# Kernel optimization log

Measured on AMD Instinct MI355X. Metric: run time of the kernel, lower is better.

The kernel has to match this reference:

```python
import math
import jax, jax.numpy as jnp
import numpy as np

DIM = 256
HEADS = 8
WS = (8, 8)   # window_size
SS = (4, 4)   # shift_size


def _rel_tables():
    """Static SwinV2 continuous relative-position coordinate table and index."""
    wh, ww = WS
    ch = np.arange(-(wh - 1), wh, dtype=np.float32)
    cw = np.arange(-(ww - 1), ww, dtype=np.float32)
    table = np.stack(np.meshgrid(ch, cw, indexing='ij'), axis=-1)  # (2wh-1, 2ww-1, 2)
    table[..., 0] /= (wh - 1)
    table[..., 1] /= (ww - 1)
    table *= 8.0
    table = np.sign(table) * np.log2(np.abs(table) + 1.0) / 3.0
    coords = np.stack(np.meshgrid(np.arange(wh), np.arange(ww), indexing='ij'))
    cf = coords.reshape(2, -1)                      # (2, N)
    rel = (cf[:, :, None] - cf[:, None, :]).transpose(1, 2, 0)  # (N, N, 2)
    rel[..., 0] += wh - 1
    rel[..., 1] += ww - 1
    rel[..., 0] *= 2 * ww - 1
    idx = rel.sum(-1).reshape(-1)                   # (N*N,)
    return jnp.asarray(table, jnp.float32), jnp.asarray(idx, jnp.int32)


def _attn_mask(pad_H, pad_W, sh, sw):
    """Static shifted-window attention mask, shape (num_windows, N, N)."""
    wh, ww = WS
    m = np.zeros((pad_H, pad_W), np.float32)
    cnt = 0
    for hs in ((0, -wh), (-wh, -sh), (-sh, None)):
        for ws_ in ((0, -ww), (-ww, -sw), (-sw, None)):
            m[hs[0]:hs[1], ws_[0]:ws_[1]] = cnt
            cnt += 1
    m = m.reshape(pad_H // wh, wh, pad_W // ww, ww).transpose(0, 2, 1, 3)
    m = m.reshape(-1, wh * ww)                      # (nW, N)
    diff = m[:, None, :] - m[:, :, None]            # (nW, N, N)
    return jnp.asarray(np.where(diff != 0, -100.0, 0.0).astype(np.float32))


def setup_inputs() -> dict:
    key = jax.random.key(0)
    ks = jax.random.split(key, 12)
    C, Hh = DIM, HEADS
    s = 0.02
    inp = {
        'x': jax.random.normal(ks[0], (16, 64, 64, C), jnp.float32),
        'Wq': jax.random.normal(ks[1], (C, C), jnp.float32) * s,
        'bq': jnp.zeros((C,), jnp.float32),
        'Wk': jax.random.normal(ks[2], (C, C), jnp.float32) * s,
        'bk': jnp.zeros((C,), jnp.float32),
        'Wv': jax.random.normal(ks[3], (C, C), jnp.float32) * s,
        'bv': jnp.zeros((C,), jnp.float32),
        'Wo': jax.random.normal(ks[4], (C, C), jnp.float32) * s,
        'bo': jnp.zeros((C,), jnp.float32),
        'logit_scale': jnp.full((Hh, 1, 1), math.log(10.0), jnp.float32),
        'cpb_w1': jax.random.normal(ks[5], (2, 512), jnp.float32) * s,
        'cpb_b1': jnp.zeros((512,), jnp.float32),
        'cpb_w2': jax.random.normal(ks[6], (512, Hh), jnp.float32) * s,
    }
    return inp


def reference(x, Wq, bq, Wk, bk, Wv, bv, Wo, bo, logit_scale, cpb_w1, cpb_b1, cpb_w2):
    B, H, W, C = x.shape
    wh, ww = WS
    hd = C // HEADS
    pad_b = (wh - H % wh) % wh
    pad_r = (ww - W % ww) % ww
    x = jnp.pad(x, ((0, 0), (0, pad_b), (0, pad_r), (0, 0)))
    pH, pW = H + pad_b, W + pad_r
    sh = 0 if wh >= pH else SS[0]
    sw = 0 if ww >= pW else SS[1]

    xs = jnp.roll(x, (-sh, -sw), axis=(1, 2))
    nW = (pH // wh) * (pW // ww)
    N = wh * ww
    # window partition -> (B*nW, N, C)
    xw = xs.reshape(B, pH // wh, wh, pW // ww, ww, C).transpose(0, 1, 3, 2, 4, 5)
    xw = xw.reshape(B * nW, N, C)

    def heads(t):
        return t.reshape(B * nW, N, HEADS, hd).transpose(0, 2, 1, 3)  # (BnW, H, N, hd)

    q = heads(xw @ Wq + bq)
    k = heads(xw @ Wk + bk)
    v = heads(xw @ Wv + bv)

    # cosine attention (F.normalize, eps=1e-12)
    qn = q / jnp.maximum(jnp.linalg.norm(q, axis=-1, keepdims=True), 1e-12)
    kn = k / jnp.maximum(jnp.linalg.norm(k, axis=-1, keepdims=True), 1e-12)
    attn = jnp.einsum('bhnd,bhmd->bhnm', qn, kn)

    scale = jnp.exp(jnp.minimum(logit_scale, math.log(100.0)))  # (HEADS,1,1)
    attn = attn * scale[None]

    table, idx = _rel_tables()
    bias = jax.nn.relu(table @ cpb_w1 + cpb_b1) @ cpb_w2        # (2wh-1, 2ww-1, HEADS)
    bias = bias.reshape(-1, HEADS)[idx].reshape(N, N, HEADS).transpose(2, 0, 1)
    attn = attn + (16.0 * jax.nn.sigmoid(bias))[None]

    if sh + sw > 0:
        mask = _attn_mask(pH, pW, sh, sw)                        # (nW, N, N)
        attn = attn.reshape(B, nW, HEADS, N, N) + mask[None, :, None]
        attn = attn.reshape(B * nW, HEADS, N, N)

    attn = jax.nn.softmax(attn, axis=-1)
    out = jnp.einsum('bhnm,bhmd->bhnd', attn, v)
    out = out.transpose(0, 2, 1, 3).reshape(B * nW, N, C)
    out = out @ Wo + bo

    out = out.reshape(B, pH // wh, pW // ww, wh, ww, C).transpose(0, 1, 3, 2, 4, 5)
    out = out.reshape(B, pH, pW, C)
    if sh + sw > 0:
        out = jnp.roll(out, (sh, sw), axis=(1, 2))
    return out[:, :H, :W, :]
```

## Files before the change

### kernel.cpp

```cpp
#include <hip/hip_runtime.h>
#include <hip/hip_bf16.h>

typedef float floatx4 __attribute__((ext_vector_type(4)));
typedef short shortx8 __attribute__((ext_vector_type(8)));
typedef short shortx4 __attribute__((ext_vector_type(4)));

#define CFENCE() asm volatile("" ::: "memory")

__device__ __forceinline__ float bf2f(short s) {
    union { unsigned u; float f; } cv;
    cv.u = ((unsigned)(unsigned short)s) << 16;
    return cv.f;
}
__device__ __forceinline__ short f2bf(float f) {
    union { float f; unsigned u; } cv; cv.f = f;
    unsigned r = (cv.u + 0x7fffu + ((cv.u >> 16) & 1u)) >> 16;
    return (short)r;
}

__global__ __launch_bounds__(256) void wtrans(const float* __restrict__ Wq,
                                              const float* __restrict__ Wk,
                                              const float* __restrict__ Wv,
                                              const float* __restrict__ Wo,
                                              short* __restrict__ wqkv_f,
                                              short* __restrict__ wo_f) {
    int gtid = blockIdx.x * 256 + threadIdx.x;
    int f = gtid >> 6, lane = gtid & 63;
    int quad = lane >> 4, l15 = lane & 15;
    if (f < 384) {
        int n16 = f >> 3, kt = f & 7;
        int n = n16 * 16 + l15, z = n >> 8, ncol = n & 255;
        const float* src = (z == 0) ? Wq : (z == 1) ? Wk : Wv;
        shortx8 s;
#pragma unroll
        for (int j = 0; j < 8; ++j)
            s[j] = f2bf(src[(size_t)(kt * 32 + quad * 8 + j) * 256 + ncol]);
        *(shortx8*)(wqkv_f + (size_t)f * 512 + lane * 8) = s;
    } else {
        int f2 = f - 384;
        int n16 = f2 >> 3, kt = f2 & 7;
        int n = n16 * 16 + l15;
        shortx8 s;
#pragma unroll
        for (int j = 0; j < 8; ++j)
            s[j] = f2bf(Wo[(size_t)(kt * 32 + quad * 8 + j) * 256 + n]);
        *(shortx8*)(wo_f + (size_t)f2 * 512 + lane * 8) = s;
    }
}

__device__ __forceinline__ float sgnlog(float x) {
    return copysignf(__log2f(fabsf(x) + 1.f) / 3.f, x);
}
__global__ __launch_bounds__(256) void bias_mlp(const float* __restrict__ ls,
                                                const float* __restrict__ w1,
                                                const float* __restrict__ b1,
                                                const float* __restrict__ w2,
                                                float* __restrict__ b225g,
                                                float* __restrict__ scaleOut) {
    int e = blockIdx.x;
    int tid = threadIdx.x, lane = tid & 63, wid = tid >> 6;
    if (e == 0 && tid < 8) scaleOut[tid] = expf(fminf(ls[tid], 4.6051701859880914f));
    int dh = e / 15 - 7, dw = e % 15 - 7;
    float t0 = sgnlog(8.f * (float)dh / 7.f);
    float t1 = sgnlog(8.f * (float)dw / 7.f);
    float acc[8];
#pragma unroll
    for (int j = 0; j < 8; ++j) acc[j] = 0.f;
#pragma unroll
    for (int s = 0; s < 2; ++s) {
        int hsm = tid + s * 256;
        float hid = fmaxf(0.f, t0 * w1[hsm] + t1 * w1[512 + hsm] + b1[hsm]);
#pragma unroll
        for (int j = 0; j < 8; ++j) acc[j] += hid * w2[hsm * 8 + j];
    }
#pragma unroll
    for (int off = 1; off < 64; off <<= 1)
#pragma unroll
        for (int j = 0; j < 8; ++j) acc[j] += __shfl_xor(acc[j], off, 64);
    __shared__ float red[4][8];
    if (lane == 0)
#pragma unroll
        for (int j = 0; j < 8; ++j) red[wid][j] = acc[j];
    __syncthreads();
    if (tid < 8)
        b225g[e * 8 + tid] = red[0][tid] + red[1][tid] + red[2][tid] + red[3][tid];
}

__global__ __launch_bounds__(256) void bias_expand(const float* __restrict__ b225g,
                                                   float* __restrict__ bias_t) {
    int f = blockIdx.x * 256 + threadIdx.x;
    int h = f >> 12, ij = f & 4095, i = ij >> 6, j = ij & 63;
    int dh = (i >> 3) - (j >> 3), dw = (i & 7) - (j & 7);
    int e = (dh + 7) * 15 + (dw + 7);
    float v = b225g[e * 8 + h];
    bias_t[(h << 12) + j * 64 + i] = 16.f / (1.f + expf(-v));
}

__device__ __forceinline__ int row2pix(int row) {
    int w = row >> 6, t = row & 63;
    int b = w >> 6, wi = (w >> 3) & 7, wj = w & 7;
    int hh = (wi * 8 + (t >> 3) + 4) & 63;
    int ww = (wj * 8 + (t & 7) + 4) & 63;
    return (b * 64 + hh) * 64 + ww;
}

__device__ __forceinline__ int regid(int t, int wi, int wj) {
    int a = (wi < 7) ? 0 : (((t >> 3) < 4) ? 1 : 2);
    int b = (wj < 7) ? 0 : (((t & 7) < 4) ? 1 : 2);
    return a * 3 + b;
}

__global__ __launch_bounds__(256) void xtrans(const float* __restrict__ x,
                                              short* __restrict__ xbf) {
    int win = blockIdx.x;
    int tid = threadIdx.x;
    int r = tid >> 2, q = tid & 3;
    const float* src = x + (size_t)row2pix(win * 64 + r) * 256 + q * 64;
    size_t fb = (size_t)(win * 4 + (r >> 4)) * 8;
    int l15r = r & 15;
#pragma unroll
    for (int kt2 = 0; kt2 < 2; ++kt2) {
        int kt = q * 2 + kt2;
        short* dst = xbf + (fb + kt) * 512 + l15r * 8;
#pragma unroll
        for (int quad = 0; quad < 4; ++quad) {
            float4 u0 = *(const float4*)(src + kt2 * 32 + quad * 8);
            float4 u1 = *(const float4*)(src + kt2 * 32 + quad * 8 + 4);
            shortx8 t;
            t[0] = f2bf(u0.x); t[1] = f2bf(u0.y); t[2] = f2bf(u0.z); t[3] = f2bf(u0.w);
            t[4] = f2bf(u1.x); t[5] = f2bf(u1.y); t[6] = f2bf(u1.z); t[7] = f2bf(u1.w);
            *(shortx8*)(dst + quad * 128) = t;
        }
    }
}

__global__ __launch_bounds__(256, 2) void swin_fused(const short* __restrict__ xbf,
                                                     const short* __restrict__ wf,
                                                     const short* __restrict__ wof,
                                                     const float* __restrict__ bq,
                                                     const float* __restrict__ bk_,
                                                     const float* __restrict__ bv,
                                                     const float* __restrict__ bo,
                                                     const float* __restrict__ bias_t,
                                                     const float* __restrict__ scale,
                                                     float* __restrict__ out) {
    __shared__ __align__(16) short lds[29696];
    int tid = threadIdx.x, lane = tid & 63, wid = tid >> 6;
    int quad = lane >> 4, l15 = lane & 15;
    int win = blockIdx.x;
    int wi = (win >> 3) & 7, wj = win & 7;
    bool need_mask = (wi == 7) || (wj == 7);

    short* qn = &lds[wid * 7424];
    short* kn = qn + 2560;
    short* vt = qn + 5120;
    short* P  = qn;

    const short* xfb = xbf + (size_t)(win * 4) * 8 * 512 + lane * 8;

    shortx4 Obf[2][4][2];

#pragma unroll
    for (int p = 0; p < 2; ++p) {
        int h = wid * 2 + p;
        floatx4 aq[2][4], ak[2][4], av[2][4];
#pragma unroll
        for (int i = 0; i < 2; ++i)
#pragma unroll
            for (int mt = 0; mt < 4; ++mt) {
                aq[i][mt] = (floatx4){0.f, 0.f, 0.f, 0.f};
                ak[i][mt] = (floatx4){0.f, 0.f, 0.f, 0.f};
                av[i][mt] = (floatx4){0.f, 0.f, 0.f, 0.f};
            }
#pragma unroll
        for (int kt = 0; kt < 8; ++kt) {
            shortx8 af[4];
#pragma unroll
            for (int mt = 0; mt < 4; ++mt)
                af[mt] = *(const shortx8*)(xfb + (size_t)(mt * 8 + kt) * 512);
            shortx8 wqf[2], wkf[2], wvf[2];
#pragma unroll
            for (int i = 0; i < 2; ++i) {
                int n16 = 2 * h + i;
                wqf[i] = *(const shortx8*)(wf + (size_t)((n16)*8 + kt) * 512 + lane * 8);
                wkf[i] = *(const shortx8*)(wf + (size_t)((16 + n16) * 8 + kt) * 512 + lane * 8);
                wvf[i] = *(const shortx8*)(wf + (size_t)((32 + n16) * 8 + kt) * 512 + lane * 8);
            }
#pragma unroll
            for (int i = 0; i < 2; ++i)
#pragma unroll
                for (int mt = 0; mt < 4; ++mt) {
                    aq[i][mt] = __builtin_amdgcn_mfma_f32_16x16x32_bf16(wqf[i], af[mt], aq[i][mt], 0, 0, 0);
                    ak[i][mt] = __builtin_amdgcn_mfma_f32_16x16x32_bf16(wkf[i], af[mt], ak[i][mt], 0, 0, 0);
                    av[i][mt] = __builtin_amdgcn_mfma_f32_16x16x32_bf16(wvf[i], af[mt], av[i][mt], 0, 0, 0);
                }
        }
        float sc = scale[h];
        float qs[4], ks[4];
#pragma unroll
        for (int mt = 0; mt < 4; ++mt) { qs[mt] = 0.f; ks[mt] = 0.f; }
#pragma unroll
        for (int i = 0; i < 2; ++i) {
            float bqv[4], bkv[4], bvv[4];
#pragma unroll
            for (int r = 0; r < 4; ++r) {
                int d = i * 16 + quad * 4 + r;
                bqv[r] = bq[h * 32 + d];
                bkv[r] = bk_[h * 32 + d];
                bvv[r] = bv[h * 32 + d];
            }
#pragma unroll
            for (int mt = 0; mt < 4; ++mt)
#pragma unroll
                for (int r = 0; r < 4; ++r) {
                    float qv = aq[i][mt][r] + bqv[r]; aq[i][mt][r] = qv; qs[mt] += qv * qv;
                    float kv = ak[i][mt][r] + bkv[r]; ak[i][mt][r] = kv; ks[mt] += kv * kv;
                    av[i][mt][r] += bvv[r];
                }
        }
#pragma unroll
        for (int mt = 0; mt < 4; ++mt) {
            qs[mt] += __shfl_xor(qs[mt], 16, 64); qs[mt] += __shfl_xor(qs[mt], 32, 64);
            ks[mt] += __shfl_xor(ks[mt], 16, 64); ks[mt] += __shfl_xor(ks[mt], 32, 64);
        }
        CFENCE();
#pragma unroll
        for (int mt = 0; mt < 4; ++mt) {
            float qr = sc / fmaxf(sqrtf(qs[mt]), 1e-12f);
            float kr = 1.f / fmaxf(sqrtf(ks[mt]), 1e-12f);
            int tok = mt * 16 + l15;
#pragma unroll
            for (int i = 0; i < 2; ++i) {
                shortx4 oq, ok;
#pragma unroll
                for (int r = 0; r < 4; ++r) {
                    oq[r] = f2bf(aq[i][mt][r] * qr);
                    ok[r] = f2bf(ak[i][mt][r] * kr);
                }
                *(shortx4*)&qn[tok * 40 + i * 16 + quad * 4] = oq;
                *(shortx4*)&kn[tok * 40 + i * 16 + quad * 4] = ok;
#pragma unroll
                for (int r = 0; r < 4; ++r)
                    vt[(i * 16 + quad * 4 + r) * 72 + tok] = f2bf(av[i][mt][r]);
            }
        }
        CFENCE();
        shortx8 aqf[4], bkf[4];
#pragma unroll
        for (int mt = 0; mt < 4; ++mt)
            aqf[mt] = *(const shortx8*)&qn[(mt * 16 + l15) * 40 + quad * 8];
#pragma unroll
        for (int nt = 0; nt < 4; ++nt)
            bkf[nt] = *(const shortx8*)&kn[(nt * 16 + l15) * 40 + quad * 8];
        floatx4 S[4][4];
#pragma unroll
        for (int mt = 0; mt < 4; ++mt)
#pragma unroll
            for (int nt = 0; nt < 4; ++nt) {
                floatx4 z = {0.f, 0.f, 0.f, 0.f};
                S[mt][nt] = __builtin_amdgcn_mfma_f32_16x16x32_bf16(aqf[mt], bkf[nt], z, 0, 0, 0);
            }
        const float* bh = bias_t + (h << 12);
        float bound = sc + 16.5f;
        int jid[4];
        if (need_mask) {
#pragma unroll
            for (int nt = 0; nt < 4; ++nt) jid[nt] = regid(nt * 16 + l15, wi, wj);
        }
        float rs[4][4];
#pragma unroll
        for (int mt = 0; mt < 4; ++mt) {
            float4 b4[4];
#pragma unroll
            for (int nt = 0; nt < 4; ++nt)
                b4[nt] = *(const float4*)&bh[(nt * 16 + l15) * 64 + mt * 16 + quad * 4];
#pragma unroll
            for (int reg = 0; reg < 4; ++reg) {
                int i = mt * 16 + quad * 4 + reg;
                int iid = need_mask ? regid(i, wi, wj) : 0;
                float rowsum = 0.f;
#pragma unroll
                for (int nt = 0; nt < 4; ++nt) {
                    float bb = (reg == 0) ? b4[nt].x : (reg == 1) ? b4[nt].y
                             : (reg == 2) ? b4[nt].z : b4[nt].w;
                    float v = S[mt][nt][reg] + bb;
                    if (need_mask && iid != jid[nt]) v -= 100.f;
                    float pe = __expf(v - bound);
                    S[mt][nt][reg] = pe;
                    rowsum += pe;
                }
                rowsum += __shfl_xor(rowsum, 1, 64);
                rowsum += __shfl_xor(rowsum, 2, 64);
                rowsum += __shfl_xor(rowsum, 4, 64);
                rowsum += __shfl_xor(rowsum, 8, 64);
                rs[mt][reg] = 1.f / rowsum;
            }
        }
        CFENCE();
#pragma unroll
        for (int mt = 0; mt < 4; ++mt)
#pragma unroll
            for (int nt = 0; nt < 4; ++nt)
#pragma unroll
                for (int reg = 0; reg < 4; ++reg)
                    P[(mt * 16 + quad * 4 + reg) * 72 + nt * 16 + l15] = f2bf(S[mt][nt][reg]);
        CFENCE();
        floatx4 O[4][2];
#pragma unroll
        for (int mt = 0; mt < 4; ++mt)
#pragma unroll
            for (int nt = 0; nt < 2; ++nt) O[mt][nt] = (floatx4){0.f, 0.f, 0.f, 0.f};
#pragma unroll
        for (int ks2 = 0; ks2 < 2; ++ks2) {
            shortx8 pa[4], vb[2];
#pragma unroll
            for (int mt = 0; mt < 4; ++mt)
                pa[mt] = *(const shortx8*)&P[(mt * 16 + l15) * 72 + ks2 * 32 + quad * 8];
#pragma unroll
            for (int nt = 0; nt < 2; ++nt)
                vb[nt] = *(const shortx8*)&vt[(nt * 16 + l15) * 72 + ks2 * 32 + quad * 8];
#pragma unroll
            for (int mt = 0; mt < 4; ++mt)
#pragma unroll
                for (int nt = 0; nt < 2; ++nt)
                    O[mt][nt] = __builtin_amdgcn_mfma_f32_16x16x32_bf16(pa[mt], vb[nt], O[mt][nt], 0, 0, 0);
        }
#pragma unroll
        for (int mt = 0; mt < 4; ++mt)
#pragma unroll
            for (int nt = 0; nt < 2; ++nt) {
                shortx4 s;
#pragma unroll
                for (int reg = 0; reg < 4; ++reg)
                    s[reg] = f2bf(O[mt][nt][reg] * rs[mt][reg]);
                Obf[p][mt][nt] = s;
            }
        CFENCE();
    }

    __syncthreads();
    short* Ao = lds;
#pragma unroll
    for (int p = 0; p < 2; ++p) {
        int h = wid * 2 + p;
#pragma unroll
        for (int mt = 0; mt < 4; ++mt)
#pragma unroll
            for (int nt = 0; nt < 2; ++nt)
#pragma unroll
                for (int reg = 0; reg < 4; ++reg)
                    Ao[(mt * 16 + quad * 4 + reg) * 264 + h * 32 + nt * 16 + l15] =
                        Obf[p][mt][nt][reg];
    }
    __syncthreads();

    int pix[4];
#pragma unroll
    for (int mt = 0; mt < 4; ++mt) pix[mt] = row2pix(win * 64 + mt * 16 + l15);

    floatx4 acc2[4][4];
#pragma unroll
    for (int nt = 0; nt < 4; ++nt)
#pragma unroll
        for (int mt = 0; mt < 4; ++mt) acc2[nt][mt] = (floatx4){0.f, 0.f, 0.f, 0.f};
#pragma unroll
    for (int kt = 0; kt < 8; ++kt) {
        shortx8 bw[4], af2[4];
#pragma unroll
        for (int nt = 0; nt < 4; ++nt)
            bw[nt] = *(const shortx8*)(wof + (size_t)((wid * 4 + nt) * 8 + kt) * 512 + lane * 8);
#pragma unroll
        for (int mt = 0; mt < 4; ++mt)
            af2[mt] = *(const shortx8*)&Ao[(mt * 16 + l15) * 264 + kt * 32 + quad * 8];
#pragma unroll
        for (int nt = 0; nt < 4; ++nt)
#pragma unroll
            for (int mt = 0; mt < 4; ++mt)
                acc2[nt][mt] = __builtin_amdgcn_mfma_f32_16x16x32_bf16(bw[nt], af2[mt], acc2[nt][mt], 0, 0, 0);
    }
#pragma unroll
    for (int nt = 0; nt < 4; ++nt) {
        int nb = wid * 64 + nt * 16 + quad * 4;
        float bs[4];
#pragma unroll
        for (int reg = 0; reg < 4; ++reg) bs[reg] = bo[nb + reg];
#pragma unroll
        for (int mt = 0; mt < 4; ++mt) {
            float4 o;
            o.x = acc2[nt][mt][0] + bs[0];
            o.y = acc2[nt][mt][1] + bs[1];
            o.z = acc2[nt][mt][2] + bs[2];
            o.w = acc2[nt][mt][3] + bs[3];
            *(float4*)(out + (size_t)pix[mt] * 256 + nb) = o;
        }
    }
}

extern "C" void kernel_launch(void* const* d_in, const int* in_sizes, int n_in,
                              void* d_out, int out_size, void* d_ws, size_t ws_size,
                              hipStream_t stream) {
    const float* x  = (const float*)d_in[0];
    const float* Wq = (const float*)d_in[1];
    const float* bq = (const float*)d_in[2];
    const float* Wk = (const float*)d_in[3];
    const float* bk = (const float*)d_in[4];
    const float* Wv = (const float*)d_in[5];
    const float* bv = (const float*)d_in[6];
    const float* Wo = (const float*)d_in[7];
    const float* bo = (const float*)d_in[8];
    const float* ls = (const float*)d_in[9];
    const float* w1 = (const float*)d_in[10];
    const float* b1 = (const float*)d_in[11];
    const float* w2 = (const float*)d_in[12];

    char* ws = (char*)d_ws;
    short* wqkv_f = (short*)(ws + 0);
    short* wo_f   = (short*)(ws + 393216);
    float* bias_t = (float*)(ws + 524288);
    float* scale  = (float*)(ws + 655360);
    float* b225g  = (float*)(ws + 786432);
    short* xbf    = (short*)(ws + 1048576);
    float* out    = (float*)d_out;

    hipLaunchKernelGGL(wtrans, dim3(128), dim3(256), 0, stream, Wq, Wk, Wv, Wo, wqkv_f, wo_f);
    hipLaunchKernelGGL(bias_mlp, dim3(225), dim3(256), 0, stream, ls, w1, b1, w2, b225g, scale);
    hipLaunchKernelGGL(bias_expand, dim3(128), dim3(256), 0, stream, b225g, bias_t);
    hipLaunchKernelGGL(xtrans, dim3(1024), dim3(256), 0, stream, x, xbf);
    hipLaunchKernelGGL(swin_fused, dim3(1024), dim3(256), 0, stream,
                       xbf, wqkv_f, wo_f, bq, bk, bv, bo, bias_t, scale, out);
}
```

Measured before the change: 238.2 us.

## Split V projection from Q/K, pack LDS in fragment order, raise occupancy

Moves the V projection into a separate pass after Q/K are normalized and stored. This cuts how many accumulators are live at once, so the launch bound can go from 2 to 3 blocks per CU. LDS tiles for q, k, v and P are repacked without padding, in MFMA fragment order, so each lane reads one contiguous 16-byte chunk. That shrinks per-block LDS enough to fit three blocks, at the cost of re-reading the x fragments from global memory for the V pass and possibly more bank conflicts on the scattered writes.

Measured after the change: 250.9 us. 5.3% more time.

```diff
diff --git a/kernel.cpp b/kernel.cpp
--- a/kernel.cpp
+++ b/kernel.cpp
@@ -134,7 +134,7 @@
     }
 }
 
-__global__ __launch_bounds__(256, 2) void swin_fused(const short* __restrict__ xbf,
+__global__ __launch_bounds__(256, 3) void swin_fused(const short* __restrict__ xbf,
                                                      const short* __restrict__ wf,
                                                      const short* __restrict__ wof,
                                                      const float* __restrict__ bq,
@@ -144,17 +144,20 @@
                                                      const float* __restrict__ bias_t,
                                                      const float* __restrict__ scale,
                                                      float* __restrict__ out) {
-    __shared__ __align__(16) short lds[29696];
+    __shared__ __align__(16) short lds[24576];
     int tid = threadIdx.x, lane = tid & 63, wid = tid >> 6;
     int quad = lane >> 4, l15 = lane & 15;
     int win = blockIdx.x;
     int wi = (win >> 3) & 7, wj = win & 7;
     bool need_mask = (wi == 7) || (wj == 7);
 
-    short* qn = &lds[wid * 7424];
-    short* kn = qn + 2560;
-    short* vt = qn + 5120;
+    short* qn = &lds[wid * 6144];
+    short* kn = qn + 2048;
+    short* vt = qn + 4096;
     short* P  = qn;
+
+    int wq2 = quad >> 1, wq1 = quad & 1;
+    int l3 = l15 >> 3, j7 = l15 & 7;
 
     const short* xfb = xbf + (size_t)(win * 4) * 8 * 512 + lane * 8;
 
@@ -163,14 +166,14 @@
 #pragma unroll
     for (int p = 0; p < 2; ++p) {
         int h = wid * 2 + p;
-        floatx4 aq[2][4], ak[2][4], av[2][4];
+        float sc = scale[h];
+        floatx4 aq[2][4], ak[2][4];
 #pragma unroll
         for (int i = 0; i < 2; ++i)
 #pragma unroll
             for (int mt = 0; mt < 4; ++mt) {
                 aq[i][mt] = (floatx4){0.f, 0.f, 0.f, 0.f};
                 ak[i][mt] = (floatx4){0.f, 0.f, 0.f, 0.f};
-                av[i][mt] = (floatx4){0.f, 0.f, 0.f, 0.f};
             }
 #pragma unroll
         for (int kt = 0; kt < 8; ++kt) {
@@ -178,13 +181,12 @@
 #pragma unroll
             for (int mt = 0; mt < 4; ++mt)
                 af[mt] = *(const shortx8*)(xfb + (size_t)(mt * 8 + kt) * 512);
-            shortx8 wqf[2], wkf[2], wvf[2];
+            shortx8 wqf[2], wkf[2];
 #pragma unroll
             for (int i = 0; i < 2; ++i) {
                 int n16 = 2 * h + i;
                 wqf[i] = *(const shortx8*)(wf + (size_t)((n16)*8 + kt) * 512 + lane * 8);
                 wkf[i] = *(const shortx8*)(wf + (size_t)((16 + n16) * 8 + kt) * 512 + lane * 8);
-                wvf[i] = *(const shortx8*)(wf + (size_t)((32 + n16) * 8 + kt) * 512 + lane * 8);
             }
 #pragma unroll
             for (int i = 0; i < 2; ++i)
@@ -192,22 +194,19 @@
                 for (int mt = 0; mt < 4; ++mt) {
                     aq[i][mt] = __builtin_amdgcn_mfma_f32_16x16x32_bf16(wqf[i], af[mt], aq[i][mt], 0, 0, 0);
                     ak[i][mt] = __builtin_amdgcn_mfma_f32_16x16x32_bf16(wkf[i], af[mt], ak[i][mt], 0, 0, 0);
-                    av[i][mt] = __builtin_amdgcn_mfma_f32_16x16x32_bf16(wvf[i], af[mt], av[i][mt], 0, 0, 0);
                 }
         }
-        float sc = scale[h];
         float qs[4], ks[4];
 #pragma unroll
         for (int mt = 0; mt < 4; ++mt) { qs[mt] = 0.f; ks[mt] = 0.f; }
 #pragma unroll
         for (int i = 0; i < 2; ++i) {
-            float bqv[4], bkv[4], bvv[4];
+            float bqv[4], bkv[4];
 #pragma unroll
             for (int r = 0; r < 4; ++r) {
                 int d = i * 16 + quad * 4 + r;
                 bqv[r] = bq[h * 32 + d];
                 bkv[r] = bk_[h * 32 + d];
-                bvv[r] = bv[h * 32 + d];
             }
 #pragma unroll
             for (int mt = 0; mt < 4; ++mt)
@@ -215,7 +214,6 @@
                 for (int r = 0; r < 4; ++r) {
                     float qv = aq[i][mt][r] + bqv[r]; aq[i][mt][r] = qv; qs[mt] += qv * qv;
                     float kv = ak[i][mt][r] + bkv[r]; ak[i][mt][r] = kv; ks[mt] += kv * kv;
-                    av[i][mt][r] += bvv[r];
                 }
         }
 #pragma unroll
@@ -228,7 +226,6 @@
         for (int mt = 0; mt < 4; ++mt) {
             float qr = sc / fmaxf(sqrtf(qs[mt]), 1e-12f);
             float kr = 1.f / fmaxf(sqrtf(ks[mt]), 1e-12f);
-            int tok = mt * 16 + l15;
 #pragma unroll
             for (int i = 0; i < 2; ++i) {
                 shortx4 oq, ok;
@@ -237,21 +234,56 @@
                     oq[r] = f2bf(aq[i][mt][r] * qr);
                     ok[r] = f2bf(ak[i][mt][r] * kr);
                 }
-                *(shortx4*)&qn[tok * 40 + i * 16 + quad * 4] = oq;
-                *(shortx4*)&kn[tok * 40 + i * 16 + quad * 4] = ok;
+                int addr = mt * 512 + (l15 + (i * 2 + wq2) * 16) * 8 + wq1 * 4;
+                *(shortx4*)&qn[addr] = oq;
+                *(shortx4*)&kn[addr] = ok;
+            }
+        }
+        CFENCE();
+        floatx4 av[2][4];
+#pragma unroll
+        for (int i = 0; i < 2; ++i)
+#pragma unroll
+            for (int mt = 0; mt < 4; ++mt) av[i][mt] = (floatx4){0.f, 0.f, 0.f, 0.f};
+#pragma unroll
+        for (int kt = 0; kt < 8; ++kt) {
+            shortx8 af[4];
+#pragma unroll
+            for (int mt = 0; mt < 4; ++mt)
+                af[mt] = *(const shortx8*)(xfb + (size_t)(mt * 8 + kt) * 512);
+            shortx8 wvf[2];
+#pragma unroll
+            for (int i = 0; i < 2; ++i) {
+                int n16 = 2 * h + i;
+                wvf[i] = *(const shortx8*)(wf + (size_t)((32 + n16) * 8 + kt) * 512 + lane * 8);
+            }
+#pragma unroll
+            for (int i = 0; i < 2; ++i)
+#pragma unroll
+                for (int mt = 0; mt < 4; ++mt)
+                    av[i][mt] = __builtin_amdgcn_mfma_f32_16x16x32_bf16(wvf[i], af[mt], av[i][mt], 0, 0, 0);
+        }
+#pragma unroll
+        for (int i = 0; i < 2; ++i) {
+            float bvv[4];
+#pragma unroll
+            for (int r = 0; r < 4; ++r) bvv[r] = bv[h * 32 + i * 16 + quad * 4 + r];
+#pragma unroll
+            for (int mt = 0; mt < 4; ++mt)
 #pragma unroll
                 for (int r = 0; r < 4; ++r)
-                    vt[(i * 16 + quad * 4 + r) * 72 + tok] = f2bf(av[i][mt][r]);
-            }
+                    vt[(i * 2 + (mt >> 1)) * 512 +
+                       (quad * 4 + r + ((mt & 1) * 2 + l3) * 16) * 8 + j7] =
+                        f2bf(av[i][mt][r] + bvv[r]);
         }
         CFENCE();
         shortx8 aqf[4], bkf[4];
 #pragma unroll
         for (int mt = 0; mt < 4; ++mt)
-            aqf[mt] = *(const shortx8*)&qn[(mt * 16 + l15) * 40 + quad * 8];
+            aqf[mt] = *(const shortx8*)&qn[mt * 512 + lane * 8];
 #pragma unroll
         for (int nt = 0; nt < 4; ++nt)
-            bkf[nt] = *(const shortx8*)&kn[(nt * 16 + l15) * 40 + quad * 8];
+            bkf[nt] = *(const shortx8*)&kn[nt * 512 + lane * 8];
         floatx4 S[4][4];
 #pragma unroll
         for (int mt = 0; mt < 4; ++mt)
@@ -303,7 +335,9 @@
             for (int nt = 0; nt < 4; ++nt)
 #pragma unroll
                 for (int reg = 0; reg < 4; ++reg)
-                    P[(mt * 16 + quad * 4 + reg) * 72 + nt * 16 + l15] = f2bf(S[mt][nt][reg]);
+                    P[(mt * 2 + (nt >> 1)) * 512 +
+                      (quad * 4 + reg + ((nt & 1) * 2 + l3) * 16) * 8 + j7] =
+                        f2bf(S[mt][nt][reg]);
         CFENCE();
         floatx4 O[4][2];
 #pragma unroll
@@ -315,10 +349,10 @@
             shortx8 pa[4], vb[2];
 #pragma unroll
             for (int mt = 0; mt < 4; ++mt)
-                pa[mt] = *(const shortx8*)&P[(mt * 16 + l15) * 72 + ks2 * 32 + quad * 8];
+                pa[mt] = *(const shortx8*)&P[(mt * 2 + ks2) * 512 + lane * 8];
 #pragma unroll
             for (int nt = 0; nt < 2; ++nt)
-                vb[nt] = *(const shortx8*)&vt[(nt * 16 + l15) * 72 + ks2 * 32 + quad * 8];
+                vb[nt] = *(const shortx8*)&vt[(nt * 2 + ks2) * 512 + lane * 8];
 #pragma unroll
             for (int mt = 0; mt < 4; ++mt)
 #pragma unroll
```
